# Kernel optimization log

Hardware: AMD Instinct MI355X
Metric: run time of the kernel (lower is better)

## Reference

```python
import jax, jax.numpy as jnp
import numpy as np

EMB = 256
N_HEADS = 8
N_LVLS = 4
N_POINTS = 4
HEAD_DIM = EMB // N_HEADS  # 32
D_FFN = 1024
SHAPES = [(100, 100), (50, 50), (25, 25), (13, 13)]
LEN = sum(h * w for h, w in SHAPES)  # 13294
B = 4


def setup_inputs() -> dict:
    key = jax.random.key(0)
    ks = jax.random.split(key, 20)
    rn = lambda k, s, sc=0.02: jax.random.normal(k, s, jnp.float32) * sc
    starts = np.cumsum([0] + [h * w for h, w in SHAPES])[:-1]
    return {
        'features': jax.random.normal(ks[0], (B, LEN, EMB), jnp.float32),
        'pos': jax.random.normal(ks[1], (B, LEN, EMB), jnp.float32),
        'reference_points': jax.random.uniform(ks[2], (B, LEN, N_LVLS, 2), jnp.float32),
        'spatial_shapes': jnp.array(SHAPES, jnp.int32),
        'lvl_start_idx': jnp.array(starts, jnp.int32),
        'W_off': rn(ks[3], (EMB, N_HEADS * N_LVLS * N_POINTS * 2)),
        'b_off': rn(ks[4], (N_HEADS * N_LVLS * N_POINTS * 2,), 0.5),
        'W_attn': rn(ks[5], (EMB, N_HEADS * N_LVLS * N_POINTS)),
        'b_attn': rn(ks[6], (N_HEADS * N_LVLS * N_POINTS,)),
        'W_val': rn(ks[7], (EMB, EMB)),
        'b_val': rn(ks[8], (EMB,)),
        'W_out': rn(ks[9], (EMB, EMB)),
        'b_out': rn(ks[10], (EMB,)),
        'ln1_g': jnp.ones((EMB,), jnp.float32),
        'ln1_b': jnp.zeros((EMB,), jnp.float32),
        'W1': rn(ks[11], (EMB, D_FFN)),
        'b1': rn(ks[12], (D_FFN,)),
        'W2': rn(ks[13], (D_FFN, EMB)),
        'b2': rn(ks[14], (EMB,)),
        'ln2_g': jnp.ones((EMB,), jnp.float32),
        'ln2_b': jnp.zeros((EMB,), jnp.float32),
    }


def _layer_norm(x, g, b, eps=1e-5):
    mu = jnp.mean(x, axis=-1, keepdims=True)
    var = jnp.mean(jnp.square(x - mu), axis=-1, keepdims=True)
    return (x - mu) * jax.lax.rsqrt(var + eps) * g + b


def _ms_deform_attn(q, features, reference_points, shapes, starts,
                    W_off, b_off, W_attn, b_attn, W_val, b_val, W_out, b_out):
    Bn, Lq, D = features.shape
    value = (features @ W_val + b_val).reshape(Bn, Lq, N_HEADS, HEAD_DIM)
    off = (q @ W_off + b_off).reshape(Bn, Lq, N_HEADS, N_LVLS, N_POINTS, 2)
    attn = (q @ W_attn + b_attn).reshape(Bn, Lq, N_HEADS, N_LVLS * N_POINTS)
    attn = jax.nn.softmax(attn, axis=-1).reshape(Bn, Lq, N_HEADS, N_LVLS, N_POINTS)
    # normalizer per level is (W, H) for (x, y)
    norm = jnp.array([[w, h] for h, w in shapes], jnp.float32)  # (L, 2)
    loc = reference_points[:, :, None, :, None, :] + off / norm[None, None, None, :, None, :]

    out = jnp.zeros((Bn, N_HEADS, Lq, HEAD_DIM), value.dtype)
    for l, (H_, W_) in enumerate(shapes):
        s = starts[l]
        val = value[:, s:s + H_ * W_].transpose(0, 2, 1, 3)  # (B, nH, HW, Dh)
        locl = loc[:, :, :, l]  # (B, Lq, nH, P, 2), in [0,1]
        # grid_sample align_corners=False convention
        x = locl[..., 0] * W_ - 0.5
        y = locl[..., 1] * H_ - 0.5
        x0 = jnp.floor(x); y0 = jnp.floor(y)
        wx = x - x0; wy = y - y0
        x0i = x0.astype(jnp.int32); y0i = y0.astype(jnp.int32)

        def corner(xi, yi, w):
            valid = (xi >= 0) & (xi < W_) & (yi >= 0) & (yi < H_)
            idx = jnp.clip(yi, 0, H_ - 1) * W_ + jnp.clip(xi, 0, W_ - 1)  # (B, Lq, nH, P)
            idx = idx.transpose(0, 2, 1, 3).reshape(Bn, N_HEADS, Lq * N_POINTS, 1)
            g = jnp.take_along_axis(val, idx, axis=2)  # (B, nH, Lq*P, Dh)
            wm = (w * valid.astype(w.dtype)).transpose(0, 2, 1, 3).reshape(Bn, N_HEADS, Lq * N_POINTS, 1)
            return g * wm

        samp = (corner(x0i, y0i, (1 - wx) * (1 - wy))
                + corner(x0i + 1, y0i, wx * (1 - wy))
                + corner(x0i, y0i + 1, (1 - wx) * wy)
                + corner(x0i + 1, y0i + 1, wx * wy))
        samp = samp.reshape(Bn, N_HEADS, Lq, N_POINTS, HEAD_DIM)
        aw = attn[:, :, :, l].transpose(0, 2, 1, 3)  # (B, nH, Lq, P)
        out = out + jnp.einsum('bhqpd,bhqp->bhqd', samp, aw)

    out = out.transpose(0, 2, 1, 3).reshape(Bn, Lq, D)
    return out @ W_out + b_out


def reference(features, pos, reference_points, spatial_shapes, lvl_start_idx,
              W_off, b_off, W_attn, b_attn, W_val, b_val, W_out, b_out,
              ln1_g, ln1_b, W1, b1, W2, b2, ln2_g, ln2_b):
    shapes = [tuple(int(v) for v in r) for r in np.asarray(spatial_shapes)]
    starts = [int(v) for v in np.asarray(lvl_start_idx)]
    q = features + pos
    attn_out = _ms_deform_attn(q, features, reference_points, shapes, starts,
                               W_off, b_off, W_attn, b_attn, W_val, b_val, W_out, b_out)
    x = _layer_norm(features + attn_out, ln1_g, ln1_b)  # dropout is identity in eval
    ffn = jax.nn.relu(x @ W1 + b1) @ W2 + b2
    x = _layer_norm(x + ffn, ln2_g, ln2_b)  # stochastic depth is identity in eval
    return x
```

## Files before the change

kernel.cpp:

```cpp
#include <hip/hip_runtime.h>
#include <stdint.h>

#define LEN_T 13294
#define M_TOK 53176

typedef unsigned short u16;
typedef __bf16 bf16x8 __attribute__((ext_vector_type(8)));
typedef float f32x4 __attribute__((ext_vector_type(4)));
typedef uint32_t u32x4 __attribute__((ext_vector_type(4)));

__device__ __forceinline__ u16 f2bf(float f) {
    union { float f; uint32_t u; } v; v.f = f;
    uint32_t r = v.u + 0x7fffu + ((v.u >> 16) & 1u);
    return (u16)(r >> 16);
}
__device__ __forceinline__ float bf2f(u16 s) {
    union { uint32_t u; float f; } v; v.u = ((uint32_t)s) << 16;
    return v.f;
}
__device__ __forceinline__ u16 f2h(float f) {
    union { _Float16 h; u16 u; } c; c.h = (_Float16)f; return c.u;
}
__device__ __forceinline__ float hlo(uint32_t u) {
    union { uint32_t u; _Float16 h[2]; } v; v.u = u; return (float)v.h[0];
}
__device__ __forceinline__ float hhi(uint32_t u) {
    union { uint32_t u; _Float16 h[2]; } v; v.u = u; return (float)v.h[1];
}

__device__ __forceinline__ void gload_lds16(const u16* g, u16* l) {
    __builtin_amdgcn_global_load_lds(
        (const __attribute__((address_space(1))) uint32_t*)(g),
        (__attribute__((address_space(3))) uint32_t*)(l), 16, 0, 0);
}

__global__ __launch_bounds__(256) void prep_qf(
    const float* __restrict__ feat, const float* __restrict__ pos,
    u16* __restrict__ qb, u16* __restrict__ fb, int n4)
{
    int i = blockIdx.x * blockDim.x + threadIdx.x;
    int stride = gridDim.x * blockDim.x;
    for (; i < n4; i += stride) {
        float4 f = ((const float4*)feat)[i];
        float4 p = ((const float4*)pos)[i];
        uint32_t q0 = (uint32_t)f2bf(f.x + p.x) | ((uint32_t)f2bf(f.y + p.y) << 16);
        uint32_t q1 = (uint32_t)f2bf(f.z + p.z) | ((uint32_t)f2bf(f.w + p.w) << 16);
        uint32_t f0 = (uint32_t)f2bf(f.x) | ((uint32_t)f2bf(f.y) << 16);
        uint32_t f1 = (uint32_t)f2bf(f.z) | ((uint32_t)f2bf(f.w) << 16);
        ((uint2*)qb)[i] = make_uint2(q0, q1);
        ((uint2*)fb)[i] = make_uint2(f0, f1);
    }
}

__global__ __launch_bounds__(256) void wtrans_all(
    const float* __restrict__ W_val, const float* __restrict__ W_off,
    const float* __restrict__ W_attn, const float* __restrict__ W_out,
    const float* __restrict__ W1, const float* __restrict__ W2,
    u16* __restrict__ Wt_val, u16* __restrict__ Wt_oa,
    u16* __restrict__ Wt_out, u16* __restrict__ W1f, u16* __restrict__ W2f)
{
    int gid = blockIdx.x * 256 + threadIdx.x;
    if (gid < 229376) {
        const float* W; u16* D; int K, N, off;
        if      (gid < 65536)  { W = W_val;  D = Wt_val;        K = 256; N = 256; off = gid; }
        else if (gid < 131072) { W = W_off;  D = Wt_oa;         K = 256; N = 256; off = gid - 65536; }
        else if (gid < 163840) { W = W_attn; D = Wt_oa + 65536; K = 256; N = 128; off = gid - 131072; }
        else                   { W = W_out;  D = Wt_out;        K = 256; N = 256; off = gid - 163840; }
        int n = off / K, k = off - n * K;
        D[off] = f2bf(W[(size_t)k * N + n]);
    } else if (gid < 491520) {
        int off = gid - 229376;
        int e = off & 7, lane = (off >> 3) & 63;
        int r = off >> 9;
        int ks = r & 7, ni = (r >> 3) & 1, c = r >> 4;
        int col = c * 32 + ni * 16 + (lane & 15);
        int k = ks * 32 + (lane >> 4) * 8 + e;
        W1f[off] = f2bf(W1[(size_t)k * 1024 + col]);
    } else if (gid < 753664) {
        int off = gid - 491520;
        int e = off & 7, lane = (off >> 3) & 63;
        int r = off >> 9;
        int col = (r & 15) * 16 + (lane & 15);
        int k = (r >> 4) * 32 + (lane >> 4) * 8 + e;
        W2f[off] = f2bf(W2[(size_t)k * 256 + col]);
    }
}

#define MODE_VAL 0
#define MODE_OFFATTN 1

template<int MODE>
__global__ __launch_bounds__(256, 2) void gemm128(
    const u16* __restrict__ A, const u16* __restrict__ Bt,
    int M, int K,
    const float* __restrict__ bias, const float* __restrict__ bias2,
    void* __restrict__ out0, void* __restrict__ out1)
{
    __shared__ u16 Al[128 * 64];
    __shared__ u16 Bl[128 * 64];
    const int tid = threadIdx.x;
    const int lane = tid & 63;
    const int w = tid >> 6;
    const int wr = w >> 1, wc = w & 1;
    const int m0 = blockIdx.x * 128;
    const int n0 = blockIdx.y * 128;
    const int l15 = lane & 15;
    const int kg = lane >> 4;
    const int srow = lane >> 3;
    const int scol = (lane & 7) * 8;

    f32x4 acc[4][4];
#pragma unroll
    for (int i = 0; i < 4; ++i)
#pragma unroll
        for (int j = 0; j < 4; ++j)
            acc[i][j] = (f32x4){0.f, 0.f, 0.f, 0.f};

    const int nk = K >> 6;
    for (int kc = 0; kc < nk; ++kc) {
        __syncthreads();
#pragma unroll
        for (int j = 0; j < 4; ++j) {
            int c = w * 4 + j;
            int arow = m0 + c * 8 + srow;
            arow = arow < M ? arow : M - 1;
            gload_lds16(A + (size_t)arow * K + (kc << 6) + scol, Al + c * 512);
            int brow = n0 + c * 8 + srow;
            gload_lds16(Bt + (size_t)brow * K + (kc << 6) + scol, Bl + c * 512);
        }
        __syncthreads();
#pragma unroll
        for (int ks = 0; ks < 2; ++ks) {
            bf16x8 af[4], bfr[4];
#pragma unroll
            for (int i = 0; i < 4; ++i) {
                af[i]  = *(const bf16x8*)(Al + (wr * 64 + i * 16 + l15) * 64 + ks * 32 + kg * 8);
                bfr[i] = *(const bf16x8*)(Bl + (wc * 64 + i * 16 + l15) * 64 + ks * 32 + kg * 8);
            }
#pragma unroll
            for (int mi = 0; mi < 4; ++mi)
#pragma unroll
                for (int ni = 0; ni < 4; ++ni)
                    acc[mi][ni] = __builtin_amdgcn_mfma_f32_16x16x32_bf16(
                        af[mi], bfr[ni], acc[mi][ni], 0, 0, 0);
        }
    }

#pragma unroll
    for (int mi = 0; mi < 4; ++mi) {
#pragma unroll
        for (int r = 0; r < 4; ++r) {
            int row = m0 + wr * 64 + mi * 16 + kg * 4 + r;
            if (row >= M) continue;
#pragma unroll
            for (int ni = 0; ni < 4; ++ni) {
                int col = n0 + wc * 64 + ni * 16 + l15;
                float v = acc[mi][ni][r];
                if (MODE == MODE_VAL) {
                    int bI = row / LEN_T;
                    int t = row - bI * LEN_T;
                    int hh = col >> 5, d = col & 31;
                    ((u16*)out0)[((size_t)(bI * 8 + hh) * LEN_T + t) * 32 + d] =
                        f2h(v + bias[col]);
                } else {
                    if (col < 256) {
                        ((u16*)out0)[((size_t)(col >> 5) * M_TOK + row) * 32 + (col & 31)] =
                            f2h(v + bias[col]);
                    } else {
                        int c = col - 256;
                        ((u16*)out1)[((size_t)(c >> 4) * M_TOK + row) * 16 + (c & 15)] =
                            f2h(v + bias2[c]);
                    }
                }
            }
        }
    }
}

template<int KSTEPS, int OUTF32>
__global__ __launch_bounds__(256, 2) void gemm_ln(
    const u16* __restrict__ A, const u16* __restrict__ Bt,
    const float* __restrict__ bias, const u16* __restrict__ res,
    const float* __restrict__ g, const float* __restrict__ bb,
    u16* __restrict__ outb, float* __restrict__ outf, int M)
{
    __shared__ char ldsraw[66560];
    u16* Al = (u16*)ldsraw;
    u16* Bl = (u16*)(ldsraw + 8192);
    float* dump = (float*)ldsraw;
    const int tid = threadIdx.x;
    const int lane = tid & 63;
    const int w = tid >> 6;
    const int l15 = lane & 15;
    const int kg = lane >> 4;
    const int srow = lane >> 3;
    const int scol = (lane & 7) * 8;
    const int m0 = blockIdx.x * 64;
    const int K = KSTEPS * 64;

    f32x4 acc[4][4];
#pragma unroll
    for (int i = 0; i < 4; ++i)
#pragma unroll
        for (int j = 0; j < 4; ++j)
            acc[i][j] = (f32x4){0.f, 0.f, 0.f, 0.f};

    for (int kc = 0; kc < KSTEPS; ++kc) {
        __syncthreads();
#pragma unroll
        for (int j = 0; j < 2; ++j) {
            int c = w * 2 + j;
            int arow = m0 + c * 8 + srow;
            arow = arow < M ? arow : M - 1;
            gload_lds16(A + (size_t)arow * K + (kc << 6) + scol, Al + c * 512);
        }
#pragma unroll
        for (int j = 0; j < 8; ++j) {
            int c = w * 8 + j;
            int brow = c * 8 + srow;
            gload_lds16(Bt + (size_t)brow * K + (kc << 6) + scol, Bl + c * 512);
        }
        __syncthreads();
#pragma unroll
        for (int ks = 0; ks < 2; ++ks) {
            bf16x8 af[4], bfr[4];
#pragma unroll
            for (int i = 0; i < 4; ++i) {
                af[i]  = *(const bf16x8*)(Al + (i * 16 + l15) * 64 + ks * 32 + kg * 8);
                bfr[i] = *(const bf16x8*)(Bl + (w * 64 + i * 16 + l15) * 64 + ks * 32 + kg * 8);
            }
#pragma unroll
            for (int mi = 0; mi < 4; ++mi)
#pragma unroll
                for (int ni = 0; ni < 4; ++ni)
                    acc[mi][ni] = __builtin_amdgcn_mfma_f32_16x16x32_bf16(
                        af[mi], bfr[ni], acc[mi][ni], 0, 0, 0);
        }
    }

    __syncthreads();
#pragma unroll
    for (int mi = 0; mi < 4; ++mi) {
#pragma unroll
        for (int r = 0; r < 4; ++r) {
            int rr = mi * 16 + kg * 4 + r;
            int gr = m0 + rr; gr = gr < M ? gr : M - 1;
#pragma unroll
            for (int ni = 0; ni < 4; ++ni) {
                int col = w * 64 + ni * 16 + l15;
                dump[rr * 260 + col] = acc[mi][ni][r] + bias[col] +
                                       bf2f(res[(size_t)gr * 256 + col]);
            }
        }
    }
    __syncthreads();

    float4 gv = *(const float4*)(g + lane * 4);
    float4 bv = *(const float4*)(bb + lane * 4);
#pragma unroll
    for (int i = 0; i < 16; ++i) {
        int rr = w * 16 + i;
        float4 x = *(const float4*)(dump + rr * 260 + lane * 4);
        float s1 = x.x + x.y + x.z + x.w;
        float s2 = x.x*x.x + x.y*x.y + x.z*x.z + x.w*x.w;
#pragma unroll
        for (int o = 1; o < 64; o <<= 1) {
            s1 += __shfl_xor(s1, o);
            s2 += __shfl_xor(s2, o);
        }
        float mu = s1 * (1.0f / 256.0f);
        float var = s2 * (1.0f / 256.0f) - mu * mu;
        float rs = rsqrtf(var + 1e-5f);
        float o0 = (x.x - mu) * rs * gv.x + bv.x;
        float o1 = (x.y - mu) * rs * gv.y + bv.y;
        float o2 = (x.z - mu) * rs * gv.z + bv.z;
        float o3 = (x.w - mu) * rs * gv.w + bv.w;
        int grow = m0 + rr;
        if (grow < M) {
            if (OUTF32) {
                *(float4*)(outf + (size_t)grow * 256 + lane * 4) =
                    make_float4(o0, o1, o2, o3);
            } else {
                uint32_t u0 = (uint32_t)f2bf(o0) | ((uint32_t)f2bf(o1) << 16);
                uint32_t u1 = (uint32_t)f2bf(o2) | ((uint32_t)f2bf(o3) << 16);
                *(uint2*)(outb + (size_t)grow * 256 + lane * 4) = make_uint2(u0, u1);
            }
        }
    }
}

__global__ __launch_bounds__(256, 2) void ffn_fused(
    const u16* __restrict__ A, const u16* __restrict__ W1f, const u16* __restrict__ W2f,
    const float* __restrict__ b1, const float* __restrict__ b2,
    const float* __restrict__ g, const float* __restrict__ bb,
    float* __restrict__ outf, int M)
{
    __shared__ char lds[66560];
    u16* Axl = (u16*)lds;
    u16* ht  = (u16*)(lds + 33792);
    float* dump = (float*)lds;
    const int tid = threadIdx.x;
    const int lane = tid & 63;
    const int w = tid >> 6;
    const int l15 = lane & 15;
    const int kg = lane >> 4;
    const int m0 = blockIdx.x * 64;

#pragma unroll
    for (int i = 0; i < 8; ++i) {
        int linear = i * 256 + tid;
        int row = linear >> 5;
        int gcol = (linear & 31) * 8;
        int grow = m0 + row; grow = grow < M ? grow : M - 1;
        uint4 v = *(const uint4*)(A + (size_t)grow * 256 + gcol);
        *(uint4*)(Axl + row * 264 + gcol) = v;
    }
    __syncthreads();

    f32x4 acc[4][4];
#pragma unroll
    for (int i = 0; i < 4; ++i)
#pragma unroll
        for (int j = 0; j < 4; ++j)
            acc[i][j] = (f32x4){0.f, 0.f, 0.f, 0.f};

    for (int hc = 0; hc < 8; ++hc) {
        f32x4 acc2[4][2];
#pragma unroll
        for (int i = 0; i < 4; ++i) {
            acc2[i][0] = (f32x4){0.f, 0.f, 0.f, 0.f};
            acc2[i][1] = (f32x4){0.f, 0.f, 0.f, 0.f};
        }
#pragma unroll
        for (int ks = 0; ks < 8; ++ks) {
            bf16x8 af[4], bw[2];
#pragma unroll
            for (int ni = 0; ni < 2; ++ni)
                bw[ni] = *(const bf16x8*)(W1f +
                    ((size_t)((((hc * 4 + w) * 2 + ni) * 8 + ks)) << 9) + lane * 8);
#pragma unroll
            for (int mi = 0; mi < 4; ++mi)
                af[mi] = *(const bf16x8*)(Axl + (mi * 16 + l15) * 264 + ks * 32 + kg * 8);
#pragma unroll
            for (int mi = 0; mi < 4; ++mi)
#pragma unroll
                for (int ni = 0; ni < 2; ++ni)
                    acc2[mi][ni] = __builtin_amdgcn_mfma_f32_16x16x32_bf16(
                        af[mi], bw[ni], acc2[mi][ni], 0, 0, 0);
        }
        __syncthreads();
#pragma unroll
        for (int mi = 0; mi < 4; ++mi) {
#pragma unroll
            for (int ni = 0; ni < 2; ++ni) {
#pragma unroll
                for (int r = 0; r < 4; ++r) {
                    int rr = mi * 16 + kg * 4 + r;
                    int cl = w * 32 + ni * 16 + l15;
                    float hv = acc2[mi][ni][r] + b1[hc * 128 + cl];
                    ht[rr * 136 + cl] = f2bf(hv > 0.f ? hv : 0.f);
                }
            }
        }
        __syncthreads();
#pragma unroll
        for (int ks2 = 0; ks2 < 4; ++ks2) {
            bf16x8 ah[4], bw2[4];
#pragma unroll
            for (int ni = 0; ni < 4; ++ni)
                bw2[ni] = *(const bf16x8*)(W2f +
                    ((size_t)(((hc * 4 + ks2) * 16 + w * 4 + ni)) << 9) + lane * 8);
#pragma unroll
            for (int mi = 0; mi < 4; ++mi)
                ah[mi] = *(const bf16x8*)(ht + (mi * 16 + l15) * 136 + ks2 * 32 + kg * 8);
#pragma unroll
            for (int mi = 0; mi < 4; ++mi)
#pragma unroll
                for (int ni = 0; ni < 4; ++ni)
                    acc[mi][ni] = __builtin_amdgcn_mfma_f32_16x16x32_bf16(
                        ah[mi], bw2[ni], acc[mi][ni], 0, 0, 0);
        }
    }

    __syncthreads();
#pragma unroll
    for (int mi = 0; mi < 4; ++mi) {
#pragma unroll
        for (int r = 0; r < 4; ++r) {
            int rr = mi * 16 + kg * 4 + r;
            int gr = m0 + rr; gr = gr < M ? gr : M - 1;
#pragma unroll
            for (int ni = 0; ni < 4; ++ni) {
                int col = w * 64 + ni * 16 + l15;
                dump[rr * 260 + col] = acc[mi][ni][r] + b2[col] +
                                       bf2f(A[(size_t)gr * 256 + col]);
            }
        }
    }
    __syncthreads();

    float4 gv = *(const float4*)(g + lane * 4);
    float4 bv = *(const float4*)(bb + lane * 4);
#pragma unroll
    for (int i = 0; i < 16; ++i) {
        int rr = w * 16 + i;
        float4 x = *(const float4*)(dump + rr * 260 + lane * 4);
        float s1 = x.x + x.y + x.z + x.w;
        float s2 = x.x*x.x + x.y*x.y + x.z*x.z + x.w*x.w;
#pragma unroll
        for (int o = 1; o < 64; o <<= 1) {
            s1 += __shfl_xor(s1, o);
            s2 += __shfl_xor(s2, o);
        }
        float mu = s1 * (1.0f / 256.0f);
        float var = s2 * (1.0f / 256.0f) - mu * mu;
        float rs = rsqrtf(var + 1e-5f);
        float o0 = (x.x - mu) * rs * gv.x + bv.x;
        float o1 = (x.y - mu) * rs * gv.y + bv.y;
        float o2 = (x.z - mu) * rs * gv.z + bv.z;
        float o3 = (x.w - mu) * rs * gv.w + bv.w;
        int grow = m0 + rr;
        if (grow < M) {
            *(float4*)(outf + (size_t)grow * 256 + lane * 4) =
                make_float4(o0, o1, o2, o3);
        }
    }
}

__device__ __forceinline__ void acc8h(u32x4 v, float w, float* acc) {
    acc[0] = fmaf(hlo(v.x), w, acc[0]);
    acc[1] = fmaf(hhi(v.x), w, acc[1]);
    acc[2] = fmaf(hlo(v.y), w, acc[2]);
    acc[3] = fmaf(hhi(v.y), w, acc[3]);
    acc[4] = fmaf(hlo(v.z), w, acc[4]);
    acc[5] = fmaf(hhi(v.z), w, acc[5]);
    acc[6] = fmaf(hlo(v.w), w, acc[6]);
    acc[7] = fmaf(hhi(v.w), w, acc[7]);
}

__global__ __launch_bounds__(256, 4) void sample_kernel(
    const u16* __restrict__ offt, const u16* __restrict__ attnt,
    const u16* __restrict__ value, const float* __restrict__ refp,
    u16* __restrict__ samp)
{
    int bid = blockIdx.x;
    int lb  = (bid & 7) * 832 + (bid >> 3);
    int bh  = lb / 208;
    int tblk = lb - bh * 208;
    int pr  = threadIdx.x >> 2;
    int dq  = threadIdx.x & 3;
    int tok = tblk * 64 + pr;
    if (tok >= LEN_T) return;
    int b = bh >> 3, h = bh & 7;
    size_t row = (size_t)b * LEN_T + tok;

    const u32x4* ap = (const u32x4*)(attnt + ((size_t)h * M_TOK + row) * 16);
    u32x4 a0 = __builtin_nontemporal_load(ap);
    u32x4 a1 = __builtin_nontemporal_load(ap + 1);
    float aw[16];
    aw[0]=hlo(a0.x); aw[1]=hhi(a0.x); aw[2]=hlo(a0.y); aw[3]=hhi(a0.y);
    aw[4]=hlo(a0.z); aw[5]=hhi(a0.z); aw[6]=hlo(a0.w); aw[7]=hhi(a0.w);
    aw[8]=hlo(a1.x); aw[9]=hhi(a1.x); aw[10]=hlo(a1.y); aw[11]=hhi(a1.y);
    aw[12]=hlo(a1.z); aw[13]=hhi(a1.z); aw[14]=hlo(a1.w); aw[15]=hhi(a1.w);
    float mx = -1e30f;
#pragma unroll
    for (int i = 0; i < 16; ++i) mx = fmaxf(mx, aw[i]);
    float ssum = 0.f;
#pragma unroll
    for (int i = 0; i < 16; ++i) { aw[i] = __expf(aw[i] - mx); ssum += aw[i]; }
    float inv = 1.0f / ssum;
#pragma unroll
    for (int i = 0; i < 16; ++i) aw[i] *= inv;

    const f32x4* rp4 = (const f32x4*)(refp + row * 8);
    f32x4 r01 = __builtin_nontemporal_load(rp4);
    f32x4 r23 = __builtin_nontemporal_load(rp4 + 1);
    float rxy[8] = {r01.x, r01.y, r01.z, r01.w, r23.x, r23.y, r23.z, r23.w};

    float acc[8];
#pragma unroll
    for (int d = 0; d < 8; ++d) acc[d] = 0.f;

    const u32x4* op4 = (const u32x4*)(offt + ((size_t)h * M_TOK + row) * 32);

    const int Wl[4] = {100, 50, 25, 13};
    const int Sl[4] = {0, 10000, 12500, 13125};

#pragma unroll
    for (int l = 0; l < 4; ++l) {
        const int W_ = Wl[l];
        const float Wf = (float)W_;
        const float invW = 1.0f / Wf;
        const u16* vb = value + ((size_t)bh * LEN_T + Sl[l]) * 32 + dq * 8;
        float rx = rxy[l*2+0], ry = rxy[l*2+1];
        u32x4 ov = __builtin_nontemporal_load(op4 + l);
        float dxs[4] = {hlo(ov.x), hlo(ov.y), hlo(ov.z), hlo(ov.w)};
        float dys[4] = {hhi(ov.x), hhi(ov.y), hhi(ov.z), hhi(ov.w)};
        float wts[16];
        int   offs[16];
#pragma unroll
        for (int p = 0; p < 4; ++p) {
            float x = fmaf(fmaf(dxs[p], invW, rx), Wf, -0.5f);
            float y = fmaf(fmaf(dys[p], invW, ry), Wf, -0.5f);
            float x0f = floorf(x), y0f = floorf(y);
            int x0 = (int)x0f, y0 = (int)y0f;
            int x1 = x0 + 1, y1 = y0 + 1;
            float wx = x - x0f, wy = y - y0f;
            float vx0 = ((unsigned)x0 < (unsigned)W_) ? 1.f : 0.f;
            float vx1 = ((unsigned)x1 < (unsigned)W_) ? 1.f : 0.f;
            float vy0 = ((unsigned)y0 < (unsigned)W_) ? 1.f : 0.f;
            float vy1 = ((unsigned)y1 < (unsigned)W_) ? 1.f : 0.f;
            int cx0 = min(max(x0, 0), W_ - 1);
            int cx1 = min(max(x1, 0), W_ - 1);
            int cy0 = min(max(y0, 0), W_ - 1);
            int cy1 = min(max(y1, 0), W_ - 1);
            float a = aw[l*4 + p];
            wts[p*4+0] = (1.f - wx) * (1.f - wy) * a * vx0 * vy0;
            wts[p*4+1] = wx * (1.f - wy) * a * vx1 * vy0;
            wts[p*4+2] = (1.f - wx) * wy * a * vx0 * vy1;
            wts[p*4+3] = wx * wy * a * vx1 * vy1;
            offs[p*4+0] = (cy0 * W_ + cx0) * 32;
            offs[p*4+1] = (cy0 * W_ + cx1) * 32;
            offs[p*4+2] = (cy1 * W_ + cx0) * 32;
            offs[p*4+3] = (cy1 * W_ + cx1) * 32;
        }
        u32x4 vv[16];
#pragma unroll
        for (int i = 0; i < 16; ++i)
            vv[i] = *(const u32x4*)(vb + offs[i]);
#pragma unroll
        for (int i = 0; i < 16; ++i)
            acc8h(vv[i], wts[i], acc);
    }
    u32x4 uo;
    uo.x = (uint32_t)f2bf(acc[0]) | ((uint32_t)f2bf(acc[1]) << 16);
    uo.y = (uint32_t)f2bf(acc[2]) | ((uint32_t)f2bf(acc[3]) << 16);
    uo.z = (uint32_t)f2bf(acc[4]) | ((uint32_t)f2bf(acc[5]) << 16);
    uo.w = (uint32_t)f2bf(acc[6]) | ((uint32_t)f2bf(acc[7]) << 16);
    __builtin_nontemporal_store(uo, (u32x4*)(samp + row * 256 + h * 32 + dq * 8));
}

extern "C" void kernel_launch(void* const* d_in, const int* in_sizes, int n_in,
                              void* d_out, int out_size, void* d_ws, size_t ws_size,
                              hipStream_t stream)
{
    const float* features = (const float*)d_in[0];
    const float* pos      = (const float*)d_in[1];
    const float* refp     = (const float*)d_in[2];
    const float* W_off  = (const float*)d_in[5];
    const float* b_off  = (const float*)d_in[6];
    const float* W_attn = (const float*)d_in[7];
    const float* b_attn = (const float*)d_in[8];
    const float* W_val  = (const float*)d_in[9];
    const float* b_val  = (const float*)d_in[10];
    const float* W_out  = (const float*)d_in[11];
    const float* b_out  = (const float*)d_in[12];
    const float* ln1_g  = (const float*)d_in[13];
    const float* ln1_b  = (const float*)d_in[14];
    const float* W1     = (const float*)d_in[15];
    const float* b1     = (const float*)d_in[16];
    const float* W2     = (const float*)d_in[17];
    const float* b2     = (const float*)d_in[18];
    const float* ln2_g  = (const float*)d_in[19];
    const float* ln2_b  = (const float*)d_in[20];
    float* out = (float*)d_out;

    char* ws = (char*)d_ws;
    size_t o = 0;
    auto alloc = [&](size_t bytes) { char* p = ws + o; o += (bytes + 255) & ~(size_t)255; return p; };
    u16* Wt_val = (u16*)alloc((size_t)256 * 256 * 2);
    u16* Wt_oa  = (u16*)alloc((size_t)384 * 256 * 2);
    u16* Wt_out = (u16*)alloc((size_t)256 * 256 * 2);
    u16* W1f    = (u16*)alloc((size_t)1024 * 256 * 2);
    u16* W2f    = (u16*)alloc((size_t)256 * 1024 * 2);
    u16* qb     = (u16*)alloc((size_t)M_TOK * 256 * 2);
    u16* fb     = (u16*)alloc((size_t)M_TOK * 256 * 2);
    char* big   = alloc((size_t)M_TOK * 1024 * 2);
    u16* value  = (u16*)big;
    u16* offt   = (u16*)(big + (size_t)M_TOK * 256 * 2);
    u16* attnt  = (u16*)(big + (size_t)M_TOK * 256 * 2 * 2);
    u16* samp = qb;
    u16* xb   = qb;

    dim3 blk(256);
    const int mb  = (M_TOK + 127) / 128;
    const int mb64 = (M_TOK + 63) / 64;

    prep_qf<<<2048, blk, 0, stream>>>(features, pos, qb, fb, M_TOK * 256 / 4);
    wtrans_all<<<2944, blk, 0, stream>>>(W_val, W_off, W_attn, W_out, W1, W2,
                                         Wt_val, Wt_oa, Wt_out, W1f, W2f);

    gemm128<MODE_VAL><<<dim3(mb, 2), blk, 0, stream>>>(
        fb, Wt_val, M_TOK, 256, b_val, nullptr, value, nullptr);
    gemm128<MODE_OFFATTN><<<dim3(mb, 3), blk, 0, stream>>>(
        qb, Wt_oa, M_TOK, 256, b_off, b_attn, offt, attnt);

    sample_kernel<<<6656, blk, 0, stream>>>(offt, attnt, value, refp, samp);

    gemm_ln<4, 0><<<mb64, blk, 0, stream>>>(
        samp, Wt_out, b_out, fb, ln1_g, ln1_b, xb, nullptr, M_TOK);

    ffn_fused<<<mb64, blk, 0, stream>>>(
        xb, W1f, W2f, b1, b2, ln2_g, ln2_b, out, M_TOK);
}
```

Measured before the change: 340.3 us.

## Double-buffer FFN hidden tile and split deform-sampling index math across lanes

The fused FFN kernel now double-buffers the hidden-activation tile in LDS. Each iteration computes the next first-layer chunk while the current chunk feeds the second GEMM, which removes one barrier-separated phase per chunk at the cost of 2 KB more LDS. The sampling kernel splits softmax and bilinear index/weight computation across the 4 lanes of each query, one level per lane, and broadcasts weights and offsets with shuffles. This removes redundant per-lane arithmetic and loads but adds many cross-lane shuffles.

```diff
diff --git a/kernel.cpp b/kernel.cpp
--- a/kernel.cpp
+++ b/kernel.cpp
@@ -7,7 +7,9 @@
 typedef unsigned short u16;
 typedef __bf16 bf16x8 __attribute__((ext_vector_type(8)));
 typedef float f32x4 __attribute__((ext_vector_type(4)));
+typedef float f32x2 __attribute__((ext_vector_type(2)));
 typedef uint32_t u32x4 __attribute__((ext_vector_type(4)));
+typedef uint32_t u32x2 __attribute__((ext_vector_type(2)));
 
 __device__ __forceinline__ u16 f2bf(float f) {
     union { float f; uint32_t u; } v; v.f = f;
@@ -295,9 +297,10 @@
     const float* __restrict__ g, const float* __restrict__ bb,
     float* __restrict__ outf, int M)
 {
-    __shared__ char lds[66560];
+    __shared__ char lds[68608];
     u16* Axl = (u16*)lds;
-    u16* ht  = (u16*)(lds + 33792);
+    u16* ht0 = (u16*)(lds + 33792);
+    u16* ht1 = (u16*)(lds + 33792 + 17408);
     float* dump = (float*)lds;
     const int tid = threadIdx.x;
     const int lane = tid & 63;
@@ -323,64 +326,62 @@
 #pragma unroll
         for (int j = 0; j < 4; ++j)
             acc[i][j] = (f32x4){0.f, 0.f, 0.f, 0.f};
-
-    for (int hc = 0; hc < 8; ++hc) {
-        f32x4 acc2[4][2];
-#pragma unroll
-        for (int i = 0; i < 4; ++i) {
-            acc2[i][0] = (f32x4){0.f, 0.f, 0.f, 0.f};
-            acc2[i][1] = (f32x4){0.f, 0.f, 0.f, 0.f};
-        }
-#pragma unroll
-        for (int ks = 0; ks < 8; ++ks) {
-            bf16x8 af[4], bw[2];
-#pragma unroll
-            for (int ni = 0; ni < 2; ++ni)
-                bw[ni] = *(const bf16x8*)(W1f +
-                    ((size_t)((((hc * 4 + w) * 2 + ni) * 8 + ks)) << 9) + lane * 8);
-#pragma unroll
-            for (int mi = 0; mi < 4; ++mi)
-                af[mi] = *(const bf16x8*)(Axl + (mi * 16 + l15) * 264 + ks * 32 + kg * 8);
-#pragma unroll
-            for (int mi = 0; mi < 4; ++mi)
-#pragma unroll
-                for (int ni = 0; ni < 2; ++ni)
-                    acc2[mi][ni] = __builtin_amdgcn_mfma_f32_16x16x32_bf16(
-                        af[mi], bw[ni], acc2[mi][ni], 0, 0, 0);
-        }
+    f32x4 acc2[4][2];
+
+#define ZERO_ACC2() \
+    _Pragma("unroll") for (int i = 0; i < 4; ++i) { \
+        acc2[i][0] = (f32x4){0.f,0.f,0.f,0.f}; acc2[i][1] = (f32x4){0.f,0.f,0.f,0.f}; }
+
+#define FFN1_CHUNK(HC) { \
+    _Pragma("unroll") for (int ks = 0; ks < 8; ++ks) { \
+        bf16x8 af[4], bw[2]; \
+        _Pragma("unroll") for (int ni = 0; ni < 2; ++ni) \
+            bw[ni] = *(const bf16x8*)(W1f + ((size_t)(((((HC) * 4 + w) * 2 + ni) * 8 + ks)) << 9) + lane * 8); \
+        _Pragma("unroll") for (int mi = 0; mi < 4; ++mi) \
+            af[mi] = *(const bf16x8*)(Axl + (mi * 16 + l15) * 264 + ks * 32 + kg * 8); \
+        _Pragma("unroll") for (int mi = 0; mi < 4; ++mi) \
+            _Pragma("unroll") for (int ni = 0; ni < 2; ++ni) \
+                acc2[mi][ni] = __builtin_amdgcn_mfma_f32_16x16x32_bf16(af[mi], bw[ni], acc2[mi][ni], 0, 0, 0); \
+    } }
+
+#define FFN2_CHUNK(HC, HTR) { \
+    _Pragma("unroll") for (int ks2 = 0; ks2 < 4; ++ks2) { \
+        bf16x8 ah[4], bw2[4]; \
+        _Pragma("unroll") for (int ni = 0; ni < 4; ++ni) \
+            bw2[ni] = *(const bf16x8*)(W2f + ((size_t)((((HC) * 4 + ks2) * 16 + w * 4 + ni)) << 9) + lane * 8); \
+        _Pragma("unroll") for (int mi = 0; mi < 4; ++mi) \
+            ah[mi] = *(const bf16x8*)((HTR) + (mi * 16 + l15) * 136 + ks2 * 32 + kg * 8); \
+        _Pragma("unroll") for (int mi = 0; mi < 4; ++mi) \
+            _Pragma("unroll") for (int ni = 0; ni < 4; ++ni) \
+                acc[mi][ni] = __builtin_amdgcn_mfma_f32_16x16x32_bf16(ah[mi], bw2[ni], acc[mi][ni], 0, 0, 0); \
+    } }
+
+#define HT_WRITE(HC, HTW) { \
+    _Pragma("unroll") for (int mi = 0; mi < 4; ++mi) \
+        _Pragma("unroll") for (int ni = 0; ni < 2; ++ni) \
+            _Pragma("unroll") for (int r = 0; r < 4; ++r) { \
+                int rr = mi * 16 + kg * 4 + r; \
+                int cl = w * 32 + ni * 16 + l15; \
+                float hv = acc2[mi][ni][r] + b1[(HC) * 128 + cl]; \
+                (HTW)[rr * 136 + cl] = f2bf(hv > 0.f ? hv : 0.f); \
+            } }
+
+    ZERO_ACC2();
+    FFN1_CHUNK(0);
+    HT_WRITE(0, ht0);
+    __syncthreads();
+
+    for (int hc = 0; hc < 7; ++hc) {
+        u16* htr = (hc & 1) ? ht1 : ht0;
+        u16* htw = (hc & 1) ? ht0 : ht1;
+        ZERO_ACC2();
+        FFN1_CHUNK(hc + 1);
+        FFN2_CHUNK(hc, htr);
         __syncthreads();
-#pragma unroll
-        for (int mi = 0; mi < 4; ++mi) {
-#pragma unroll
-            for (int ni = 0; ni < 2; ++ni) {
-#pragma unroll
-                for (int r = 0; r < 4; ++r) {
-                    int rr = mi * 16 + kg * 4 + r;
-                    int cl = w * 32 + ni * 16 + l15;
-                    float hv = acc2[mi][ni][r] + b1[hc * 128 + cl];
-                    ht[rr * 136 + cl] = f2bf(hv > 0.f ? hv : 0.f);
-                }
-            }
-        }
+        HT_WRITE(hc + 1, htw);
         __syncthreads();
-#pragma unroll
-        for (int ks2 = 0; ks2 < 4; ++ks2) {
-            bf16x8 ah[4], bw2[4];
-#pragma unroll
-            for (int ni = 0; ni < 4; ++ni)
-                bw2[ni] = *(const bf16x8*)(W2f +
-                    ((size_t)(((hc * 4 + ks2) * 16 + w * 4 + ni)) << 9) + lane * 8);
-#pragma unroll
-            for (int mi = 0; mi < 4; ++mi)
-                ah[mi] = *(const bf16x8*)(ht + (mi * 16 + l15) * 136 + ks2 * 32 + kg * 8);
-#pragma unroll
-            for (int mi = 0; mi < 4; ++mi)
-#pragma unroll
-                for (int ni = 0; ni < 4; ++ni)
-                    acc[mi][ni] = __builtin_amdgcn_mfma_f32_16x16x32_bf16(
-                        ah[mi], bw2[ni], acc[mi][ni], 0, 0, 0);
-        }
-    }
+    }
+    FFN2_CHUNK(7, ht1);
 
     __syncthreads();
 #pragma unroll
@@ -452,85 +453,88 @@
     int tok = tblk * 64 + pr;
     if (tok >= LEN_T) return;
     int b = bh >> 3, h = bh & 7;
+    int lane = threadIdx.x & 63;
     size_t row = (size_t)b * LEN_T + tok;
 
-    const u32x4* ap = (const u32x4*)(attnt + ((size_t)h * M_TOK + row) * 16);
-    u32x4 a0 = __builtin_nontemporal_load(ap);
-    u32x4 a1 = __builtin_nontemporal_load(ap + 1);
-    float aw[16];
-    aw[0]=hlo(a0.x); aw[1]=hhi(a0.x); aw[2]=hlo(a0.y); aw[3]=hhi(a0.y);
-    aw[4]=hlo(a0.z); aw[5]=hhi(a0.z); aw[6]=hlo(a0.w); aw[7]=hhi(a0.w);
-    aw[8]=hlo(a1.x); aw[9]=hhi(a1.x); aw[10]=hlo(a1.y); aw[11]=hhi(a1.y);
-    aw[12]=hlo(a1.z); aw[13]=hhi(a1.z); aw[14]=hlo(a1.w); aw[15]=hhi(a1.w);
-    float mx = -1e30f;
-#pragma unroll
-    for (int i = 0; i < 16; ++i) mx = fmaxf(mx, aw[i]);
-    float ssum = 0.f;
-#pragma unroll
-    for (int i = 0; i < 16; ++i) { aw[i] = __expf(aw[i] - mx); ssum += aw[i]; }
-    float inv = 1.0f / ssum;
-#pragma unroll
-    for (int i = 0; i < 16; ++i) aw[i] *= inv;
-
-    const f32x4* rp4 = (const f32x4*)(refp + row * 8);
-    f32x4 r01 = __builtin_nontemporal_load(rp4);
-    f32x4 r23 = __builtin_nontemporal_load(rp4 + 1);
-    float rxy[8] = {r01.x, r01.y, r01.z, r01.w, r23.x, r23.y, r23.z, r23.w};
+    int W_    = dq == 0 ? 100 : dq == 1 ? 50 : dq == 2 ? 25 : 13;
+    float Wf   = dq == 0 ? 100.f : dq == 1 ? 50.f : dq == 2 ? 25.f : 13.f;
+    float invW = dq == 0 ? 0.01f : dq == 1 ? 0.02f : dq == 2 ? 0.04f : (1.0f / 13.0f);
+
+    u32x2 av = __builtin_nontemporal_load(
+        (const u32x2*)(attnt + ((size_t)h * M_TOK + row) * 16 + dq * 4));
+    float e0 = hlo(av.x), e1 = hhi(av.x), e2 = hlo(av.y), e3 = hhi(av.y);
+    float m = fmaxf(fmaxf(e0, e1), fmaxf(e2, e3));
+    m = fmaxf(m, __shfl_xor(m, 1));
+    m = fmaxf(m, __shfl_xor(m, 2));
+    e0 = __expf(e0 - m); e1 = __expf(e1 - m);
+    e2 = __expf(e2 - m); e3 = __expf(e3 - m);
+    float s = e0 + e1 + e2 + e3;
+    s += __shfl_xor(s, 1);
+    s += __shfl_xor(s, 2);
+    float inv = 1.0f / s;
+    float awp[4] = {e0 * inv, e1 * inv, e2 * inv, e3 * inv};
+
+    f32x2 rv = __builtin_nontemporal_load((const f32x2*)(refp + row * 8 + dq * 2));
+    float rx = rv.x, ry = rv.y;
+    u32x4 ov = __builtin_nontemporal_load(
+        (const u32x4*)(offt + ((size_t)h * M_TOK + row) * 32 + dq * 8));
+    float dxs[4] = {hlo(ov.x), hlo(ov.y), hlo(ov.z), hlo(ov.w)};
+    float dys[4] = {hhi(ov.x), hhi(ov.y), hhi(ov.z), hhi(ov.w)};
+
+    float wts[16]; int offs[16];
+#pragma unroll
+    for (int p = 0; p < 4; ++p) {
+        float x = fmaf(fmaf(dxs[p], invW, rx), Wf, -0.5f);
+        float y = fmaf(fmaf(dys[p], invW, ry), Wf, -0.5f);
+        float x0f = floorf(x), y0f = floorf(y);
+        int x0 = (int)x0f, y0 = (int)y0f;
+        int x1 = x0 + 1, y1 = y0 + 1;
+        float wx = x - x0f, wy = y - y0f;
+        float vx0 = ((unsigned)x0 < (unsigned)W_) ? 1.f : 0.f;
+        float vx1 = ((unsigned)x1 < (unsigned)W_) ? 1.f : 0.f;
+        float vy0 = ((unsigned)y0 < (unsigned)W_) ? 1.f : 0.f;
+        float vy1 = ((unsigned)y1 < (unsigned)W_) ? 1.f : 0.f;
+        int cx0 = min(max(x0, 0), W_ - 1);
+        int cx1 = min(max(x1, 0), W_ - 1);
+        int cy0 = min(max(y0, 0), W_ - 1);
+        int cy1 = min(max(y1, 0), W_ - 1);
+        float a = awp[p];
+        wts[p*4+0] = (1.f - wx) * (1.f - wy) * a * vx0 * vy0;
+        wts[p*4+1] = wx * (1.f - wy) * a * vx1 * vy0;
+        wts[p*4+2] = (1.f - wx) * wy * a * vx0 * vy1;
+        wts[p*4+3] = wx * wy * a * vx1 * vy1;
+        offs[p*4+0] = (cy0 * W_ + cx0) * 32;
+        offs[p*4+1] = (cy0 * W_ + cx1) * 32;
+        offs[p*4+2] = (cy1 * W_ + cx0) * 32;
+        offs[p*4+3] = (cy1 * W_ + cx1) * 32;
+    }
 
     float acc[8];
 #pragma unroll
     for (int d = 0; d < 8; ++d) acc[d] = 0.f;
-
-    const u32x4* op4 = (const u32x4*)(offt + ((size_t)h * M_TOK + row) * 32);
-
-    const int Wl[4] = {100, 50, 25, 13};
-    const int Sl[4] = {0, 10000, 12500, 13125};
-
-#pragma unroll
-    for (int l = 0; l < 4; ++l) {
-        const int W_ = Wl[l];
-        const float Wf = (float)W_;
-        const float invW = 1.0f / Wf;
-        const u16* vb = value + ((size_t)bh * LEN_T + Sl[l]) * 32 + dq * 8;
-        float rx = rxy[l*2+0], ry = rxy[l*2+1];
-        u32x4 ov = __builtin_nontemporal_load(op4 + l);
-        float dxs[4] = {hlo(ov.x), hlo(ov.y), hlo(ov.z), hlo(ov.w)};
-        float dys[4] = {hhi(ov.x), hhi(ov.y), hhi(ov.z), hhi(ov.w)};
-        float wts[16];
-        int   offs[16];
-#pragma unroll
-        for (int p = 0; p < 4; ++p) {
-            float x = fmaf(fmaf(dxs[p], invW, rx), Wf, -0.5f);
-            float y = fmaf(fmaf(dys[p], invW, ry), Wf, -0.5f);
-            float x0f = floorf(x), y0f = floorf(y);
-            int x0 = (int)x0f, y0 = (int)y0f;
-            int x1 = x0 + 1, y1 = y0 + 1;
-            float wx = x - x0f, wy = y - y0f;
-            float vx0 = ((unsigned)x0 < (unsigned)W_) ? 1.f : 0.f;
-            float vx1 = ((unsigned)x1 < (unsigned)W_) ? 1.f : 0.f;
-            float vy0 = ((unsigned)y0 < (unsigned)W_) ? 1.f : 0.f;
-            float vy1 = ((unsigned)y1 < (unsigned)W_) ? 1.f : 0.f;
-            int cx0 = min(max(x0, 0), W_ - 1);
-            int cx1 = min(max(x1, 0), W_ - 1);
-            int cy0 = min(max(y0, 0), W_ - 1);
-            int cy1 = min(max(y1, 0), W_ - 1);
-            float a = aw[l*4 + p];
-            wts[p*4+0] = (1.f - wx) * (1.f - wy) * a * vx0 * vy0;
-            wts[p*4+1] = wx * (1.f - wy) * a * vx1 * vy0;
-            wts[p*4+2] = (1.f - wx) * wy * a * vx0 * vy1;
-            wts[p*4+3] = wx * wy * a * vx1 * vy1;
-            offs[p*4+0] = (cy0 * W_ + cx0) * 32;
-            offs[p*4+1] = (cy0 * W_ + cx1) * 32;
-            offs[p*4+2] = (cy1 * W_ + cx0) * 32;
-            offs[p*4+3] = (cy1 * W_ + cx1) * 32;
-        }
-        u32x4 vv[16];
-#pragma unroll
-        for (int i = 0; i < 16; ++i)
-            vv[i] = *(const u32x4*)(vb + offs[i]);
-#pragma unroll
-        for (int i = 0; i < 16; ++i)
-            acc8h(vv[i], wts[i], acc);
+    const int qbase = lane & ~3;
+
+#pragma unroll
+    for (int l2 = 0; l2 < 4; ++l2) {
+        const int SL2 = (l2 == 0) ? 0 : (l2 == 1) ? 10000 : (l2 == 2) ? 12500 : 13125;
+        const u16* vb = value + ((size_t)bh * LEN_T + SL2) * 32 + dq * 8;
+        const int src = qbase + l2;
+#pragma unroll
+        for (int c2 = 0; c2 < 2; ++c2) {
+            float w8[8]; int o8[8];
+#pragma unroll
+            for (int i = 0; i < 8; ++i) {
+                w8[i] = __shfl(wts[c2*8 + i], src);
+                o8[i] = __shfl(offs[c2*8 + i], src);
+            }
+            u32x4 vv[8];
+#pragma unroll
+            for (int i = 0; i < 8; ++i)
+                vv[i] = *(const u32x4*)(vb + o8[i]);
+#pragma unroll
+            for (int i = 0; i < 8; ++i)
+                acc8h(vv[i], w8[i], acc);
+        }
     }
     u32x4 uo;
     uo.x = (uint32_t)f2bf(acc[0]) | ((uint32_t)f2bf(acc[1]) << 16);
```

Measured after the change: 336.5 us. About the same (-1.1%).
